# Optimization experiments

Measured on AMD Instinct MI355X. Metric: run time of the kernel, lower is better.

Reference implementation:

```python
import jax, jax.numpy as jnp
import numpy as np

N_NODES = 8192
N_EDGES = 262144
D_IN = 512
D_OUT = 512


def setup_inputs() -> dict:
    key = jax.random.key(0)
    k1, k2, k3 = jax.random.split(key, 3)
    x = jax.random.normal(k1, (N_NODES, D_IN), dtype=jnp.float32)
    edge_index = jax.random.randint(k2, (2, N_EDGES), 0, N_NODES, dtype=jnp.int64)
    weight = jax.random.normal(k3, (D_IN, D_OUT), dtype=jnp.float32)
    bias = jnp.zeros((D_OUT,), dtype=jnp.float32)
    return {"x": x, "edge_index": edge_index, "weight": weight, "bias": bias}


def reference(x, edge_index, weight, bias):
    # GCN layer with selfloop=True branch of the original module.
    n = x.shape[0]
    # Dense symmetric adjacency via scatter-set, matching adj[ei0,ei1]=1; adj[ei1,ei0]=1
    adj = jnp.zeros((n, n), dtype=x.dtype)
    adj = adj.at[edge_index[0], edge_index[1]].set(1.0)
    adj = adj.at[edge_index[1], edge_index[0]].set(1.0)
    # Add self loops, symmetric degree normalization D^{-1/2} A D^{-1/2}
    adj = adj + jnp.eye(n, dtype=x.dtype)
    deg = jnp.sum(adj, axis=1)
    dinv = 1.0 / jnp.sqrt(deg)
    adj = adj * dinv[:, None] * dinv[None, :]  # == D @ adj @ D (diagonal scaling)
    return adj @ (x @ weight) + bias
```

## Files before the change

kernel.cpp:

```cpp
#include <hip/hip_runtime.h>
#include <hip/hip_bf16.h>


#define ELL_STRIDE 128

typedef __attribute__((ext_vector_type(8))) short bf16x8;
typedef __attribute__((ext_vector_type(4))) float f32x4;

__device__ __forceinline__ unsigned short f2bf(float f) {
  unsigned u = __float_as_uint(f);
  u = (u + 0x7fff + ((u >> 16) & 1)) >> 16;
  return (unsigned short)u;
}
__device__ __forceinline__ float bflo(unsigned u) {
  return __uint_as_float(u << 16);
}
__device__ __forceinline__ float bfhi(unsigned u) {
  return __uint_as_float(u & 0xffff0000u);
}

__global__ __launch_bounds__(256) void fused_front_kernel(
    const int* __restrict__ ei, unsigned* __restrict__ mask, int n_edges,
    int words,
    const float* __restrict__ x, unsigned short* __restrict__ xb, int n4,
    const float* __restrict__ W, unsigned short* __restrict__ Wt, int K, int N,
    int edge_blocks, int cast_blocks) {
  const int bid = blockIdx.x;
  if (bid < edge_blocks) {
    const int e = bid * 256 + threadIdx.x;
    if (e < n_edges) {
      const int u = ei[e];
      const int v = ei[e + n_edges];
      atomicOr(&mask[(size_t)u * words + (v >> 5)], 1u << (v & 31));
      atomicOr(&mask[(size_t)v * words + (u >> 5)], 1u << (u & 31));
    }
    return;
  }
  if (bid < edge_blocks + cast_blocks) {
    const int t = (bid - edge_blocks) * 256 + threadIdx.x;
    if (t < n4) {
      float4 v = ((const float4*)x)[t];
      ushort4 o;
      o.x = f2bf(v.x); o.y = f2bf(v.y); o.z = f2bf(v.z); o.w = f2bf(v.w);
      ((ushort4*)xb)[t] = o;
    }
    return;
  }
  {
    __shared__ float tile[32][33];
    const int b = bid - edge_blocks - cast_blocks;
    const int bx = b & ((N >> 5) - 1);
    const int by = b >> (31 - __builtin_clz(N >> 5));
    const int tx = threadIdx.x & 31;
    const int ty = threadIdx.x >> 5;
#pragma unroll
    for (int r = 0; r < 4; ++r)
      tile[ty + 8 * r][tx] = W[(size_t)(by * 32 + ty + 8 * r) * N + bx * 32 + tx];
    __syncthreads();
#pragma unroll
    for (int r = 0; r < 4; ++r)
      Wt[(size_t)(bx * 32 + ty + 8 * r) * K + by * 32 + tx] =
          f2bf(tile[tx][ty + 8 * r]);
  }
}

__global__ __launch_bounds__(256) void build_ell_kernel(
    const unsigned* __restrict__ mask, unsigned short* __restrict__ ell,
    int* __restrict__ deg, float* __restrict__ dinv, int n, int words) {
  int gtid = blockIdx.x * blockDim.x + threadIdx.x;
  int node = gtid >> 6;
  int lane = threadIdx.x & 63;
  if (node >= n) return;
  const unsigned* __restrict__ row = mask + (size_t)node * words;
  unsigned short* __restrict__ out = ell + (size_t)node * ELL_STRIDE;

  int running = 0;
  for (int r = 0; r < words; r += 64) {
    const int w = r + lane;
    unsigned bits = row[w];
    const int cnt = __popc(bits);
    int x = cnt;
#pragma unroll
    for (int d = 1; d < 64; d <<= 1) {
      int y = __shfl_up(x, d, 64);
      if (lane >= d) x += y;
    }
    int pos = running + x - cnt;
    while (bits) {
      const int b = __builtin_ctz(bits);
      bits &= bits - 1;
      if (pos < ELL_STRIDE) out[pos] = (unsigned short)((w << 5) + b);
      ++pos;
    }
    running += __shfl(x, 63, 64);
  }
  if (lane == 0) {
    deg[node] = running < ELL_STRIDE ? running : ELL_STRIDE;
    dinv[node] = rsqrtf((float)running + 1.0f);
  }
}

__global__ __launch_bounds__(256) void gemm_mfma_kernel(
    const unsigned short* __restrict__ xb,
    const unsigned short* __restrict__ Wt,
    const float* __restrict__ dinv,
    unsigned short* __restrict__ Hs,
    int M, int N, int K) {
  __shared__ unsigned short As[256 * 8];
  __shared__ unsigned short Bs[256 * 8];

  const int tid = threadIdx.x;
  const int wave = tid >> 6;
  const int lane = tid & 63;
  const int q = lane >> 4;
  const int c = lane & 15;
  const int m0 = blockIdx.y * 64;
  const int n0 = blockIdx.x * 64;
  const int wr = wave >> 1, wc = wave & 1;

  f32x4 acc[2][2] = {};

  for (int k0 = 0; k0 < K; k0 += 32) {
    {
      const int s = tid;
      const unsigned short* g = xb + (size_t)(m0 + (s & 63)) * K + k0 + (s >> 6) * 8;
      __builtin_amdgcn_global_load_lds(
          (const __attribute__((address_space(1))) void*)g,
          (__attribute__((address_space(3))) void*)(As + wave * 64 * 8), 16, 0, 0);
    }
    {
      const int s = tid;
      const unsigned short* g = Wt + (size_t)(n0 + (s >> 2)) * K + k0 + (s & 3) * 8;
      __builtin_amdgcn_global_load_lds(
          (const __attribute__((address_space(1))) void*)g,
          (__attribute__((address_space(3))) void*)(Bs + wave * 64 * 8), 16, 0, 0);
    }
    __syncthreads();

    bf16x8 a[2], b[2];
#pragma unroll
    for (int tm = 0; tm < 2; ++tm) {
      const int row = wr * 32 + tm * 16 + c;
      a[tm] = *(const bf16x8*)(As + (q * 64 + row) * 8);
    }
#pragma unroll
    for (int tn = 0; tn < 2; ++tn) {
      const int n = wc * 32 + tn * 16 + c;
      b[tn] = *(const bf16x8*)(Bs + (n * 4 + q) * 8);
    }
#pragma unroll
    for (int tm = 0; tm < 2; ++tm)
#pragma unroll
      for (int tn = 0; tn < 2; ++tn)
        acc[tm][tn] = __builtin_amdgcn_mfma_f32_16x16x32_bf16(
            a[tm], b[tn], acc[tm][tn], 0, 0, 0);
    __syncthreads();
  }

#pragma unroll
  for (int tm = 0; tm < 2; ++tm) {
#pragma unroll
    for (int r = 0; r < 4; ++r) {
      const int grow = m0 + wr * 32 + tm * 16 + q * 4 + r;
      const float di = dinv[grow];
#pragma unroll
      for (int tn = 0; tn < 2; ++tn) {
        const int gcol = n0 + wc * 32 + tn * 16 + c;
        Hs[(size_t)grow * N + gcol] = f2bf(di * acc[tm][tn][r]);
      }
    }
  }
}

__global__ __launch_bounds__(256) void spmm_kernel(
    const unsigned short* __restrict__ ell, const int* __restrict__ deg,
    const unsigned short* __restrict__ Hs, const float* __restrict__ dinv,
    const float* __restrict__ bias, float* __restrict__ out, int n, int D) {
  __shared__ unsigned short jl[4][ELL_STRIDE];
  const int wave = threadIdx.x >> 6, lane = threadIdx.x & 63;
  const int i = blockIdx.x * 4 + wave;

  jl[wave][lane] = ell[(size_t)i * ELL_STRIDE + lane];
  jl[wave][64 + lane] = ell[(size_t)i * ELL_STRIDE + 64 + lane];
  const int d = deg[i];

  const unsigned short* __restrict__ hb = Hs + lane * 8;
  float acc[8] = {0.f, 0.f, 0.f, 0.f, 0.f, 0.f, 0.f, 0.f};
#pragma unroll 8
  for (int k = 0; k < d; ++k) {
    const int j = jl[wave][k];
    const uint4 h = *(const uint4*)(hb + (size_t)j * D);
    acc[0] += bflo(h.x); acc[1] += bfhi(h.x);
    acc[2] += bflo(h.y); acc[3] += bfhi(h.y);
    acc[4] += bflo(h.z); acc[5] += bfhi(h.z);
    acc[6] += bflo(h.w); acc[7] += bfhi(h.w);
  }

  const uint4 hs = *(const uint4*)(hb + (size_t)i * D);
  acc[0] += bflo(hs.x); acc[1] += bfhi(hs.x);
  acc[2] += bflo(hs.y); acc[3] += bfhi(hs.y);
  acc[4] += bflo(hs.z); acc[5] += bfhi(hs.z);
  acc[6] += bflo(hs.w); acc[7] += bfhi(hs.w);

  const float di = dinv[i];
  const float4 b0 = *(const float4*)(bias + lane * 8);
  const float4 b1 = *(const float4*)(bias + lane * 8 + 4);
  float4 o0, o1;
  o0.x = di * acc[0] + b0.x; o0.y = di * acc[1] + b0.y;
  o0.z = di * acc[2] + b0.z; o0.w = di * acc[3] + b0.w;
  o1.x = di * acc[4] + b1.x; o1.y = di * acc[5] + b1.y;
  o1.z = di * acc[6] + b1.z; o1.w = di * acc[7] + b1.w;
  *(float4*)(out + (size_t)i * D + lane * 8) = o0;
  *(float4*)(out + (size_t)i * D + lane * 8 + 4) = o1;
}

extern "C" void kernel_launch(void* const* d_in, const int* in_sizes, int n_in,
                              void* d_out, int out_size, void* d_ws, size_t ws_size,
                              hipStream_t stream) {
  const float* x    = (const float*)d_in[0];
  const int*   ei   = (const int*)d_in[1];
  const float* W    = (const float*)d_in[2];
  const float* bias = (const float*)d_in[3];
  float* out = (float*)d_out;

  const int d_out_dim = in_sizes[3];
  const int d_in_dim  = in_sizes[2] / d_out_dim;
  const int n_nodes   = in_sizes[0] / d_in_dim;
  const int n_edges   = in_sizes[1] / 2;
  const int words     = (n_nodes + 31) / 32;

  char* ws = (char*)d_ws;
  size_t off = 0;
  unsigned* mask = (unsigned*)(ws + off); off += (size_t)n_nodes * words * 4;
  float* dinv    = (float*)(ws + off);    off += (size_t)n_nodes * 4;
  int* deg       = (int*)(ws + off);      off += (size_t)n_nodes * 4;
  unsigned short* ell = (unsigned short*)(ws + off); off += (size_t)n_nodes * ELL_STRIDE * 2;
  unsigned short* xb  = (unsigned short*)(ws + off); off += (size_t)n_nodes * d_in_dim * 2;
  unsigned short* Wt  = (unsigned short*)(ws + off); off += (size_t)d_in_dim * d_out_dim * 2;
  unsigned short* Hs  = (unsigned short*)(ws + off); off += (size_t)n_nodes * d_out_dim * 2;

  hipMemsetAsync(mask, 0, (size_t)n_nodes * words * sizeof(unsigned), stream);

  const int edge_blocks = (n_edges + 255) / 256;
  const int n4 = n_nodes * d_in_dim / 4;
  const int cast_blocks = (n4 + 255) / 256;
  const int tr_blocks = (d_in_dim / 32) * (d_out_dim / 32);
  fused_front_kernel<<<edge_blocks + cast_blocks + tr_blocks, 256, 0, stream>>>(
      ei, mask, n_edges, words, x, xb, n4, W, Wt, d_in_dim, d_out_dim,
      edge_blocks, cast_blocks);

  build_ell_kernel<<<(n_nodes * 64 + 255) / 256, 256, 0, stream>>>(
      mask, ell, deg, dinv, n_nodes, words);

  dim3 ggrid(d_out_dim / 64, n_nodes / 64);
  gemm_mfma_kernel<<<ggrid, 256, 0, stream>>>(xb, Wt, dinv, Hs,
                                              n_nodes, d_out_dim, d_in_dim);

  spmm_kernel<<<n_nodes / 4, 256, 0, stream>>>(ell, deg, Hs, dinv, bias, out,
                                               n_nodes, d_out_dim);
}
```

Measured before the change: 158.3 us.

## Count degrees during edge scatter and fuse GEMM with ELL build

Degrees are now counted during the edge scatter: an atomicAdd fires only when the atomicOr actually sets a new bit. This lets the GEMM compute dinv directly and removes its dependency on the ELL build, so the two are merged into one launch that runs side by side. The SpMM splits the feature dimension across two grid halves and has each wave's half-lanes process alternate neighbors, padding odd counts with a zeroed dummy row. The cost is extra atomics in the scatter kernel and a cross-lane shuffle reduction in the SpMM.

```diff
diff --git a/kernel.cpp b/kernel.cpp
--- a/kernel.cpp
+++ b/kernel.cpp
@@ -20,19 +20,24 @@
 }
 
 __global__ __launch_bounds__(256) void fused_front_kernel(
-    const int* __restrict__ ei, unsigned* __restrict__ mask, int n_edges,
-    int words,
+    const int* __restrict__ ei, unsigned* __restrict__ mask,
+    int* __restrict__ degcnt, int n_edges, int words,
     const float* __restrict__ x, unsigned short* __restrict__ xb, int n4,
     const float* __restrict__ W, unsigned short* __restrict__ Wt, int K, int N,
-    int edge_blocks, int cast_blocks) {
+    unsigned short* __restrict__ Hs, int n_nodes,
+    int edge_blocks, int cast_blocks, int tr_blocks) {
   const int bid = blockIdx.x;
   if (bid < edge_blocks) {
     const int e = bid * 256 + threadIdx.x;
     if (e < n_edges) {
       const int u = ei[e];
       const int v = ei[e + n_edges];
-      atomicOr(&mask[(size_t)u * words + (v >> 5)], 1u << (v & 31));
-      atomicOr(&mask[(size_t)v * words + (u >> 5)], 1u << (u & 31));
+      const unsigned bv = 1u << (v & 31);
+      const unsigned bu = 1u << (u & 31);
+      const unsigned o0 = atomicOr(&mask[(size_t)u * words + (v >> 5)], bv);
+      if (!(o0 & bv)) atomicAdd(&degcnt[u], 1);
+      const unsigned o1 = atomicOr(&mask[(size_t)v * words + (u >> 5)], bu);
+      if (!(o1 & bu)) atomicAdd(&degcnt[v], 1);
     }
     return;
   }
@@ -46,7 +51,7 @@
     }
     return;
   }
-  {
+  if (bid < edge_blocks + cast_blocks + tr_blocks) {
     __shared__ float tile[32][33];
     const int b = bid - edge_blocks - cast_blocks;
     const int bx = b & ((N >> 5) - 1);
@@ -61,157 +66,180 @@
     for (int r = 0; r < 4; ++r)
       Wt[(size_t)(bx * 32 + ty + 8 * r) * K + by * 32 + tx] =
           f2bf(tile[tx][ty + 8 * r]);
-  }
-}
-
-__global__ __launch_bounds__(256) void build_ell_kernel(
-    const unsigned* __restrict__ mask, unsigned short* __restrict__ ell,
-    int* __restrict__ deg, float* __restrict__ dinv, int n, int words) {
-  int gtid = blockIdx.x * blockDim.x + threadIdx.x;
-  int node = gtid >> 6;
-  int lane = threadIdx.x & 63;
-  if (node >= n) return;
-  const unsigned* __restrict__ row = mask + (size_t)node * words;
-  unsigned short* __restrict__ out = ell + (size_t)node * ELL_STRIDE;
-
-  int running = 0;
-  for (int r = 0; r < words; r += 64) {
-    const int w = r + lane;
-    unsigned bits = row[w];
-    const int cnt = __popc(bits);
-    int x = cnt;
-#pragma unroll
-    for (int d = 1; d < 64; d <<= 1) {
-      int y = __shfl_up(x, d, 64);
-      if (lane >= d) x += y;
-    }
-    int pos = running + x - cnt;
-    while (bits) {
-      const int b = __builtin_ctz(bits);
-      bits &= bits - 1;
-      if (pos < ELL_STRIDE) out[pos] = (unsigned short)((w << 5) + b);
-      ++pos;
-    }
-    running += __shfl(x, 63, 64);
-  }
-  if (lane == 0) {
-    deg[node] = running < ELL_STRIDE ? running : ELL_STRIDE;
-    dinv[node] = rsqrtf((float)running + 1.0f);
-  }
-}
-
-__global__ __launch_bounds__(256) void gemm_mfma_kernel(
+    return;
+  }
+  {
+    const int t = threadIdx.x;
+    if (t < (N >> 1)) ((unsigned*)(Hs + (size_t)n_nodes * N))[t] = 0;
+  }
+}
+
+__global__ __launch_bounds__(256) void fused_mid_kernel(
     const unsigned short* __restrict__ xb,
     const unsigned short* __restrict__ Wt,
-    const float* __restrict__ dinv,
+    const int* __restrict__ degcnt,
     unsigned short* __restrict__ Hs,
-    int M, int N, int K) {
+    const unsigned* __restrict__ mask, unsigned short* __restrict__ ell,
+    int M, int N, int K, int words, int gemm_blocks, int nbx_sh) {
   __shared__ unsigned short As[256 * 8];
   __shared__ unsigned short Bs[256 * 8];
 
   const int tid = threadIdx.x;
-  const int wave = tid >> 6;
-  const int lane = tid & 63;
-  const int q = lane >> 4;
-  const int c = lane & 15;
-  const int m0 = blockIdx.y * 64;
-  const int n0 = blockIdx.x * 64;
-  const int wr = wave >> 1, wc = wave & 1;
-
-  f32x4 acc[2][2] = {};
-
-  for (int k0 = 0; k0 < K; k0 += 32) {
-    {
-      const int s = tid;
-      const unsigned short* g = xb + (size_t)(m0 + (s & 63)) * K + k0 + (s >> 6) * 8;
-      __builtin_amdgcn_global_load_lds(
-          (const __attribute__((address_space(1))) void*)g,
-          (__attribute__((address_space(3))) void*)(As + wave * 64 * 8), 16, 0, 0);
-    }
-    {
-      const int s = tid;
-      const unsigned short* g = Wt + (size_t)(n0 + (s >> 2)) * K + k0 + (s & 3) * 8;
-      __builtin_amdgcn_global_load_lds(
-          (const __attribute__((address_space(1))) void*)g,
-          (__attribute__((address_space(3))) void*)(Bs + wave * 64 * 8), 16, 0, 0);
-    }
-    __syncthreads();
-
-    bf16x8 a[2], b[2];
+  const int bid = blockIdx.x;
+
+  if (bid < gemm_blocks) {
+    const int wave = tid >> 6;
+    const int lane = tid & 63;
+    const int q = lane >> 4;
+    const int c = lane & 15;
+    const int bx = bid & ((1 << nbx_sh) - 1);
+    const int by = bid >> nbx_sh;
+    const int m0 = by * 64;
+    const int n0 = bx * 64;
+    const int wr = wave >> 1, wc = wave & 1;
+
+    f32x4 acc[2][2] = {};
+
+    for (int k0 = 0; k0 < K; k0 += 32) {
+      {
+        const unsigned short* g =
+            xb + (size_t)(m0 + lane) * K + k0 + wave * 8;
+        __builtin_amdgcn_global_load_lds(
+            (const __attribute__((address_space(1))) void*)g,
+            (__attribute__((address_space(3))) void*)(As + wave * 64 * 8), 16, 0, 0);
+      }
+      {
+        const int s = tid;
+        const unsigned short* g =
+            Wt + (size_t)(n0 + (s >> 2)) * K + k0 + (s & 3) * 8;
+        __builtin_amdgcn_global_load_lds(
+            (const __attribute__((address_space(1))) void*)g,
+            (__attribute__((address_space(3))) void*)(Bs + wave * 64 * 8), 16, 0, 0);
+      }
+      __syncthreads();
+
+      bf16x8 a[2], b[2];
+#pragma unroll
+      for (int tm = 0; tm < 2; ++tm) {
+        const int row = wr * 32 + tm * 16 + c;
+        a[tm] = *(const bf16x8*)(As + (q * 64 + row) * 8);
+      }
+#pragma unroll
+      for (int tn = 0; tn < 2; ++tn) {
+        const int n = wc * 32 + tn * 16 + c;
+        b[tn] = *(const bf16x8*)(Bs + (n * 4 + q) * 8);
+      }
+#pragma unroll
+      for (int tm = 0; tm < 2; ++tm)
+#pragma unroll
+        for (int tn = 0; tn < 2; ++tn)
+          acc[tm][tn] = __builtin_amdgcn_mfma_f32_16x16x32_bf16(
+              a[tm], b[tn], acc[tm][tn], 0, 0, 0);
+      __syncthreads();
+    }
+
 #pragma unroll
     for (int tm = 0; tm < 2; ++tm) {
-      const int row = wr * 32 + tm * 16 + c;
-      a[tm] = *(const bf16x8*)(As + (q * 64 + row) * 8);
-    }
-#pragma unroll
-    for (int tn = 0; tn < 2; ++tn) {
-      const int n = wc * 32 + tn * 16 + c;
-      b[tn] = *(const bf16x8*)(Bs + (n * 4 + q) * 8);
-    }
-#pragma unroll
-    for (int tm = 0; tm < 2; ++tm)
-#pragma unroll
-      for (int tn = 0; tn < 2; ++tn)
-        acc[tm][tn] = __builtin_amdgcn_mfma_f32_16x16x32_bf16(
-            a[tm], b[tn], acc[tm][tn], 0, 0, 0);
-    __syncthreads();
-  }
-
-#pragma unroll
-  for (int tm = 0; tm < 2; ++tm) {
-#pragma unroll
-    for (int r = 0; r < 4; ++r) {
-      const int grow = m0 + wr * 32 + tm * 16 + q * 4 + r;
-      const float di = dinv[grow];
-#pragma unroll
-      for (int tn = 0; tn < 2; ++tn) {
-        const int gcol = n0 + wc * 32 + tn * 16 + c;
-        Hs[(size_t)grow * N + gcol] = f2bf(di * acc[tm][tn][r]);
-      }
+#pragma unroll
+      for (int r = 0; r < 4; ++r) {
+        const int grow = m0 + wr * 32 + tm * 16 + q * 4 + r;
+        const float di = rsqrtf((float)degcnt[grow] + 1.0f);
+#pragma unroll
+        for (int tn = 0; tn < 2; ++tn) {
+          const int gcol = n0 + wc * 32 + tn * 16 + c;
+          Hs[(size_t)grow * N + gcol] = f2bf(di * acc[tm][tn][r]);
+        }
+      }
+    }
+    return;
+  }
+
+  {
+    const int wave = tid >> 6, lane = tid & 63;
+    const int node = (bid - gemm_blocks) * 4 + wave;
+    const unsigned* __restrict__ row = mask + (size_t)node * words;
+    unsigned short* __restrict__ out = ell + (size_t)node * ELL_STRIDE;
+
+    int running = 0;
+    for (int r = 0; r < words; r += 64) {
+      const int w = r + lane;
+      unsigned bits = row[w];
+      const int cnt = __popc(bits);
+      int x = cnt;
+#pragma unroll
+      for (int d = 1; d < 64; d <<= 1) {
+        int y = __shfl_up(x, d, 64);
+        if (lane >= d) x += y;
+      }
+      int pos = running + x - cnt;
+      while (bits) {
+        const int b = __builtin_ctz(bits);
+        bits &= bits - 1;
+        if (pos < ELL_STRIDE) out[pos] = (unsigned short)((w << 5) + b);
+        ++pos;
+      }
+      running += __shfl(x, 63, 64);
+    }
+    if (lane == 0) {
+      if (running < ELL_STRIDE) out[running] = (unsigned short)M;
+      if (running + 1 < ELL_STRIDE) out[running + 1] = (unsigned short)M;
     }
   }
 }
 
 __global__ __launch_bounds__(256) void spmm_kernel(
-    const unsigned short* __restrict__ ell, const int* __restrict__ deg,
-    const unsigned short* __restrict__ Hs, const float* __restrict__ dinv,
-    const float* __restrict__ bias, float* __restrict__ out, int n, int D) {
+    const unsigned short* __restrict__ ell, const int* __restrict__ degcnt,
+    const unsigned short* __restrict__ Hs, const float* __restrict__ bias,
+    float* __restrict__ out, int n, int D) {
   __shared__ unsigned short jl[4][ELL_STRIDE];
   const int wave = threadIdx.x >> 6, lane = threadIdx.x & 63;
   const int i = blockIdx.x * 4 + wave;
+  const int h = blockIdx.y;
+  const int side = lane >> 5, hl = lane & 31;
+  const int Dh = D >> 1;
 
   jl[wave][lane] = ell[(size_t)i * ELL_STRIDE + lane];
   jl[wave][64 + lane] = ell[(size_t)i * ELL_STRIDE + 64 + lane];
-  const int d = deg[i];
-
-  const unsigned short* __restrict__ hb = Hs + lane * 8;
+  const int dc = degcnt[i];
+  const int d = dc < ELL_STRIDE ? dc : ELL_STRIDE;
+  const int kmax = (d + 1) & ~1;
+
+  const unsigned short* __restrict__ hb = Hs + h * Dh + hl * 8;
   float acc[8] = {0.f, 0.f, 0.f, 0.f, 0.f, 0.f, 0.f, 0.f};
+
+  {
+    const int js = side ? n : i;
+    const uint4 hv = *(const uint4*)(hb + (size_t)js * D);
+    acc[0] += bflo(hv.x); acc[1] += bfhi(hv.x);
+    acc[2] += bflo(hv.y); acc[3] += bfhi(hv.y);
+    acc[4] += bflo(hv.z); acc[5] += bfhi(hv.z);
+    acc[6] += bflo(hv.w); acc[7] += bfhi(hv.w);
+  }
 #pragma unroll 8
-  for (int k = 0; k < d; ++k) {
-    const int j = jl[wave][k];
-    const uint4 h = *(const uint4*)(hb + (size_t)j * D);
-    acc[0] += bflo(h.x); acc[1] += bfhi(h.x);
-    acc[2] += bflo(h.y); acc[3] += bfhi(h.y);
-    acc[4] += bflo(h.z); acc[5] += bfhi(h.z);
-    acc[6] += bflo(h.w); acc[7] += bfhi(h.w);
-  }
-
-  const uint4 hs = *(const uint4*)(hb + (size_t)i * D);
-  acc[0] += bflo(hs.x); acc[1] += bfhi(hs.x);
-  acc[2] += bflo(hs.y); acc[3] += bfhi(hs.y);
-  acc[4] += bflo(hs.z); acc[5] += bfhi(hs.z);
-  acc[6] += bflo(hs.w); acc[7] += bfhi(hs.w);
-
-  const float di = dinv[i];
-  const float4 b0 = *(const float4*)(bias + lane * 8);
-  const float4 b1 = *(const float4*)(bias + lane * 8 + 4);
-  float4 o0, o1;
-  o0.x = di * acc[0] + b0.x; o0.y = di * acc[1] + b0.y;
-  o0.z = di * acc[2] + b0.z; o0.w = di * acc[3] + b0.w;
-  o1.x = di * acc[4] + b1.x; o1.y = di * acc[5] + b1.y;
-  o1.z = di * acc[6] + b1.z; o1.w = di * acc[7] + b1.w;
-  *(float4*)(out + (size_t)i * D + lane * 8) = o0;
-  *(float4*)(out + (size_t)i * D + lane * 8 + 4) = o1;
+  for (int k = 0; k < kmax; k += 2) {
+    const int j = jl[wave][k + side];
+    const uint4 hv = *(const uint4*)(hb + (size_t)j * D);
+    acc[0] += bflo(hv.x); acc[1] += bfhi(hv.x);
+    acc[2] += bflo(hv.y); acc[3] += bfhi(hv.y);
+    acc[4] += bflo(hv.z); acc[5] += bfhi(hv.z);
+    acc[6] += bflo(hv.w); acc[7] += bfhi(hv.w);
+  }
+#pragma unroll
+  for (int t = 0; t < 8; ++t) acc[t] += __shfl_xor(acc[t], 32, 64);
+
+  if (side == 0) {
+    const float di = rsqrtf((float)dc + 1.0f);
+    const float4 b0 = *(const float4*)(bias + h * Dh + hl * 8);
+    const float4 b1 = *(const float4*)(bias + h * Dh + hl * 8 + 4);
+    float* op = out + (size_t)i * D + h * Dh + hl * 8;
+    float4 o0, o1;
+    o0.x = di * acc[0] + b0.x; o0.y = di * acc[1] + b0.y;
+    o0.z = di * acc[2] + b0.z; o0.w = di * acc[3] + b0.w;
+    o1.x = di * acc[4] + b1.x; o1.y = di * acc[5] + b1.y;
+    o1.z = di * acc[6] + b1.z; o1.w = di * acc[7] + b1.w;
+    *(float4*)op = o0;
+    *(float4*)(op + 4) = o1;
+  }
 }
 
 extern "C" void kernel_launch(void* const* d_in, const int* in_sizes, int n_in,
@@ -232,30 +260,32 @@
   char* ws = (char*)d_ws;
   size_t off = 0;
   unsigned* mask = (unsigned*)(ws + off); off += (size_t)n_nodes * words * 4;
-  float* dinv    = (float*)(ws + off);    off += (size_t)n_nodes * 4;
-  int* deg       = (int*)(ws + off);      off += (size_t)n_nodes * 4;
+  int* degcnt    = (int*)(ws + off);      off += (size_t)n_nodes * 4;
   unsigned short* ell = (unsigned short*)(ws + off); off += (size_t)n_nodes * ELL_STRIDE * 2;
   unsigned short* xb  = (unsigned short*)(ws + off); off += (size_t)n_nodes * d_in_dim * 2;
   unsigned short* Wt  = (unsigned short*)(ws + off); off += (size_t)d_in_dim * d_out_dim * 2;
-  unsigned short* Hs  = (unsigned short*)(ws + off); off += (size_t)n_nodes * d_out_dim * 2;
-
-  hipMemsetAsync(mask, 0, (size_t)n_nodes * words * sizeof(unsigned), stream);
+  unsigned short* Hs  = (unsigned short*)(ws + off);
+  off += (size_t)(n_nodes + 1) * d_out_dim * 2;
+
+  hipMemsetAsync(mask, 0, (size_t)n_nodes * words * 4 + (size_t)n_nodes * 4, stream);
 
   const int edge_blocks = (n_edges + 255) / 256;
   const int n4 = n_nodes * d_in_dim / 4;
   const int cast_blocks = (n4 + 255) / 256;
   const int tr_blocks = (d_in_dim / 32) * (d_out_dim / 32);
-  fused_front_kernel<<<edge_blocks + cast_blocks + tr_blocks, 256, 0, stream>>>(
-      ei, mask, n_edges, words, x, xb, n4, W, Wt, d_in_dim, d_out_dim,
-      edge_blocks, cast_blocks);
-
-  build_ell_kernel<<<(n_nodes * 64 + 255) / 256, 256, 0, stream>>>(
-      mask, ell, deg, dinv, n_nodes, words);
-
-  dim3 ggrid(d_out_dim / 64, n_nodes / 64);
-  gemm_mfma_kernel<<<ggrid, 256, 0, stream>>>(xb, Wt, dinv, Hs,
-                                              n_nodes, d_out_dim, d_in_dim);
-
-  spmm_kernel<<<n_nodes / 4, 256, 0, stream>>>(ell, deg, Hs, dinv, bias, out,
-                                               n_nodes, d_out_dim);
-}
+  fused_front_kernel<<<edge_blocks + cast_blocks + tr_blocks + 1, 256, 0, stream>>>(
+      ei, mask, degcnt, n_edges, words, x, xb, n4, W, Wt, d_in_dim, d_out_dim,
+      Hs, n_nodes, edge_blocks, cast_blocks, tr_blocks);
+
+  const int nbx = d_out_dim / 64;
+  const int nbx_sh = 31 - __builtin_clz(nbx);
+  const int gemm_blocks = nbx * (n_nodes / 64);
+  const int ell_blocks = n_nodes / 4;
+  fused_mid_kernel<<<gemm_blocks + ell_blocks, 256, 0, stream>>>(
+      xb, Wt, degcnt, Hs, mask, ell,
+      n_nodes, d_out_dim, d_in_dim, words, gemm_blocks, nbx_sh);
+
+  dim3 sgrid(n_nodes / 4, 2);
+  spmm_kernel<<<sgrid, 256, 0, stream>>>(ell, degcnt, Hs, bias, out,
+                                         n_nodes, d_out_dim);
+}
```

Measured after the change: 168.0 us. 6.1% more time.
